# Kernel optimization log

Measured on AMD Instinct MI355X. Metric: run time of the kernel, lower is better.

Reference implementation:

```python
import jax, jax.numpy as jnp
import numpy as np

NEG_SLOPE = 0.2


def _gat_layer(x, W, a_src, a_dst, b, src, dst, n_nodes, heads, dim):
    # x: [N, F_in]; W: [F_in, heads*dim]
    h = (x @ W).reshape(n_nodes, heads, dim)            # [N,H,D]
    e_src = (h * a_src).sum(-1)                          # [N,H]
    e_dst = (h * a_dst).sum(-1)                          # [N,H]
    e = jax.nn.leaky_relu(e_src[src] + e_dst[dst], NEG_SLOPE)  # [E,H]
    # edge softmax over incoming edges of each target node
    m = jax.ops.segment_max(e, dst, num_segments=n_nodes)      # [N,H]
    ex = jnp.exp(e - m[dst])
    denom = jax.ops.segment_sum(ex, dst, num_segments=n_nodes)  # [N,H]
    alpha = ex / denom[dst]                              # [E,H]
    out = jax.ops.segment_sum(h[src] * alpha[:, :, None], dst,
                              num_segments=n_nodes)      # [N,H,D]
    return out.reshape(n_nodes, heads * dim) + b


def setup_inputs() -> dict:
    key = jax.random.key(0)
    ks = jax.random.split(key, 10)
    N, E, F_in = 100000, 1600000, 300
    x = jax.random.normal(ks[0], (N, F_in), dtype=jnp.float32)
    edge_index = jax.random.randint(ks[1], (2, E), 0, N, dtype=jnp.int64)
    s = 0.1
    return {
        'x': x,
        'edge_index': edge_index,
        'W1': jax.random.normal(ks[2], (F_in, 64), jnp.float32) * s,
        'att_src1': jax.random.normal(ks[3], (8, 8), jnp.float32) * s,
        'att_dst1': jax.random.normal(ks[4], (8, 8), jnp.float32) * s,
        'b1': jax.random.normal(ks[5], (64,), jnp.float32) * s,
        'W2': jax.random.normal(ks[6], (64, 64), jnp.float32) * s,
        'att_src2': jax.random.normal(ks[7], (1, 64), jnp.float32) * s,
        'att_dst2': jax.random.normal(ks[8], (1, 64), jnp.float32) * s,
        'b2': jax.random.normal(ks[9], (64,), jnp.float32) * s,
    }


def reference(x, edge_index, W1, att_src1, att_dst1, b1, W2, att_src2, att_dst2, b2):
    N = x.shape[0]
    # add self-loops (PyG GATConv default)
    loop = jnp.arange(N, dtype=edge_index.dtype)
    src = jnp.concatenate([edge_index[0], loop])
    dst = jnp.concatenate([edge_index[1], loop])
    # dropout p=0.6 is identity in eval mode
    h = _gat_layer(x, W1, att_src1, att_dst1, b1, src, dst, N, 8, 8)    # [N,64]
    h = jax.nn.elu(h)
    h = _gat_layer(h, W2, att_src2, att_dst2, b2, src, dst, N, 1, 64)   # [N,64]
    return jax.nn.log_softmax(h, axis=1)
```

## Files before the change

### kernel.cpp

```cpp
#include <hip/hip_runtime.h>
#include <math.h>

using short8  = __attribute__((ext_vector_type(8))) short;
using ushort8 = __attribute__((ext_vector_type(8))) unsigned short;
using f32x4   = __attribute__((ext_vector_type(4))) float;

#define NBLKS 512
#define BPAD  800
#define EB 8

__device__ __forceinline__ unsigned short f2bf(float f) {
    unsigned u = __float_as_uint(f);
    unsigned r = u + 0x7FFF + ((u >> 16) & 1);
    return (unsigned short)(r >> 16);
}
__device__ __forceinline__ float bf2f(unsigned short v) {
    return __uint_as_float((unsigned)v << 16);
}


__global__ void detect64_kernel(const int* __restrict__ ei, int E, int* __restrict__ flag) {
    __shared__ int any;
    if (threadIdx.x == 0) any = 0;
    __syncthreads();
    for (int i = threadIdx.x; i < 1024; i += 256) {
        if (ei[2 * i + 1] != 0) { any = 1; break; }
    }
    __syncthreads();
    if (threadIdx.x == 0) *flag = (any ? 0 : 1);
}


__global__ __launch_bounds__(256) void binA_kernel(
    const int* __restrict__ ei, int E, int N, const int* __restrict__ flag,
    int nbuck, int* __restrict__ hist, int chunk) {
    __shared__ int lh[BPAD];
    for (int i = threadIdx.x; i < nbuck; i += 256) lh[i] = 0;
    __syncthreads();
    int is64 = *flag;
    int Etot = E + N;
    int beg = blockIdx.x * chunk, end = min(Etot, beg + chunk);
    for (int i = beg + threadIdx.x; i < end; i += 256) {
        int d = (i < E) ? (is64 ? ei[2 * (E + i)] : ei[E + i]) : (i - E);
        atomicAdd(&lh[d >> 7], 1);
    }
    __syncthreads();
    for (int i = threadIdx.x; i < nbuck; i += 256) hist[blockIdx.x * BPAD + i] = lh[i];
}

__global__ void scanBlocks_kernel(int* __restrict__ hist, int nbuck, int* __restrict__ bucketTotal) {
    int bin = blockIdx.x * 256 + threadIdx.x;
    if (bin >= nbuck) return;
    int run = 0;
    for (int b = 0; b < NBLKS; b++) {
        int v = hist[b * BPAD + bin];
        hist[b * BPAD + bin] = run;
        run += v;
    }
    bucketTotal[bin] = run;
}

__global__ void scanBucket_kernel(const int* __restrict__ bucketTotal, int nbuck,
                                  int* __restrict__ bucketBase) {
    __shared__ int s[1024];
    int t = threadIdx.x;
    int v = (t < nbuck) ? bucketTotal[t] : 0;
    s[t] = v;
    __syncthreads();
    for (int off = 1; off < 1024; off <<= 1) {
        int x = (t >= off) ? s[t - off] : 0;
        __syncthreads();
        s[t] += x;
        __syncthreads();
    }
    if (t < nbuck) bucketBase[t] = s[t] - v;
    if (t == nbuck - 1) bucketBase[nbuck] = s[t];
}

__global__ __launch_bounds__(256) void binB_kernel(
    const int* __restrict__ ei, int E, int N, const int* __restrict__ flag,
    int nbuck, const int* __restrict__ hist, const int* __restrict__ bucketBase,
    int* __restrict__ tmp, int chunk) {
    __shared__ int cur[BPAD];
    for (int i = threadIdx.x; i < nbuck; i += 256)
        cur[i] = bucketBase[i] + hist[blockIdx.x * BPAD + i];
    __syncthreads();
    int is64 = *flag;
    int Etot = E + N;
    int beg = blockIdx.x * chunk, end = min(Etot, beg + chunk);
    for (int i = beg + threadIdx.x; i < end; i += 256) {
        int s, d;
        if (i < E) {
            if (is64) { s = ei[2 * i]; d = ei[2 * (E + i)]; }
            else      { s = ei[i];     d = ei[E + i]; }
        } else { s = i - E; d = i - E; }
        int pos = atomicAdd(&cur[d >> 7], 1);
        tmp[pos] = ((d & 127) << 17) | s;
    }
}

__global__ __launch_bounds__(256) void binC_kernel(
    const int* __restrict__ tmp, const int* __restrict__ bucketBase, int nbuck,
    int N, int Etot, int* __restrict__ rowptr, int* __restrict__ col) {
    __shared__ int lh[128];
    __shared__ int cur[128];
    int g = blockIdx.x;
    int t = threadIdx.x;
    int beg = bucketBase[g], end = bucketBase[g + 1];
    if (t < 128) lh[t] = 0;
    __syncthreads();
    for (int i = beg + t; i < end; i += 256) atomicAdd(&lh[tmp[i] >> 17], 1);
    __syncthreads();
    int c = (t < 128) ? lh[t] : 0;
    for (int off = 1; off < 128; off <<= 1) {
        int x = 0;
        if (t < 128 && t >= off) x = lh[t - off];
        __syncthreads();
        if (t < 128) lh[t] += x;
        __syncthreads();
    }
    if (t < 128) {
        int excl = lh[t] - c;
        cur[t] = beg + excl;
        int node = g * 128 + t;
        if (node < N) rowptr[node] = beg + excl;
    }
    if (g == 0 && t == 0) rowptr[N] = Etot;
    if (g == 0 && t < 16) col[Etot + t] = 0;
    __syncthreads();
    for (int i = beg + t; i < end; i += 256) {
        int v = tmp[i];
        int pos = atomicAdd(&cur[v >> 17], 1);
        col[pos] = v & 0x1FFFF;
    }
}


__global__ __launch_bounds__(256) void gemm1_mfma_kernel(
    const float* __restrict__ x, const float* __restrict__ W,
    const float* __restrict__ asrc, const float* __restrict__ adst,
    unsigned short* __restrict__ hbf, float* __restrict__ es, float* __restrict__ ed, int N) {
    __shared__ __align__(16) unsigned short A_lds[128 * 40];
    __shared__ __align__(16) unsigned short B_lds[64 * 40];
    const int tx = threadIdx.x;
    const int wv = tx >> 6;
    const int lane = tx & 63;
    const int l15 = lane & 15;
    const int quad = lane >> 4;
    const int rowBase = blockIdx.x * 128;

    f32x4 acc[2][4];
#pragma unroll
    for (int rt = 0; rt < 2; rt++)
#pragma unroll
        for (int ct = 0; ct < 4; ct++) acc[rt][ct] = (f32x4){0.f, 0.f, 0.f, 0.f};

    const int kq = tx & 7;
    const int r0 = tx >> 3;
    const int colB = tx & 63;
    const int kkb = (tx >> 6) * 8;

    for (int k0 = 0; k0 < 320; k0 += 32) {
        bool kvalid = (k0 + kq * 4 + 4 <= 300);
#pragma unroll
        for (int p = 0; p < 4; p++) {
            int row = p * 32 + r0;
            int grow = rowBase + row;
            float4 v = make_float4(0.f, 0.f, 0.f, 0.f);
            if (kvalid && grow < N) v = *(const float4*)&x[(size_t)grow * 300 + k0 + kq * 4];
            *(ushort4*)&A_lds[row * 40 + kq * 4] =
                make_ushort4(f2bf(v.x), f2bf(v.y), f2bf(v.z), f2bf(v.w));
        }
        {
            unsigned short t0, t1, t2, t3, t4, t5, t6, t7;
            float v;
            v = (k0 + kkb + 0 < 300) ? W[(size_t)(k0 + kkb + 0) * 64 + colB] : 0.f; t0 = f2bf(v);
            v = (k0 + kkb + 1 < 300) ? W[(size_t)(k0 + kkb + 1) * 64 + colB] : 0.f; t1 = f2bf(v);
            v = (k0 + kkb + 2 < 300) ? W[(size_t)(k0 + kkb + 2) * 64 + colB] : 0.f; t2 = f2bf(v);
            v = (k0 + kkb + 3 < 300) ? W[(size_t)(k0 + kkb + 3) * 64 + colB] : 0.f; t3 = f2bf(v);
            v = (k0 + kkb + 4 < 300) ? W[(size_t)(k0 + kkb + 4) * 64 + colB] : 0.f; t4 = f2bf(v);
            v = (k0 + kkb + 5 < 300) ? W[(size_t)(k0 + kkb + 5) * 64 + colB] : 0.f; t5 = f2bf(v);
            v = (k0 + kkb + 6 < 300) ? W[(size_t)(k0 + kkb + 6) * 64 + colB] : 0.f; t6 = f2bf(v);
            v = (k0 + kkb + 7 < 300) ? W[(size_t)(k0 + kkb + 7) * 64 + colB] : 0.f; t7 = f2bf(v);
            *(ushort4*)&B_lds[colB * 40 + kkb]     = make_ushort4(t0, t1, t2, t3);
            *(ushort4*)&B_lds[colB * 40 + kkb + 4] = make_ushort4(t4, t5, t6, t7);
        }
        __syncthreads();
        short8 af[2], bfr[4];
#pragma unroll
        for (int rt = 0; rt < 2; rt++)
            af[rt] = *(const short8*)&A_lds[(wv * 32 + rt * 16 + l15) * 40 + quad * 8];
#pragma unroll
        for (int ct = 0; ct < 4; ct++)
            bfr[ct] = *(const short8*)&B_lds[(ct * 16 + l15) * 40 + quad * 8];
#pragma unroll
        for (int rt = 0; rt < 2; rt++)
#pragma unroll
            for (int ct = 0; ct < 4; ct++)
                acc[rt][ct] = __builtin_amdgcn_mfma_f32_16x16x32_bf16(af[rt], bfr[ct], acc[rt][ct], 0, 0, 0);
        __syncthreads();
    }

    float as_v[4], ad_v[4];
#pragma unroll
    for (int ct = 0; ct < 4; ct++) {
        as_v[ct] = asrc[ct * 16 + l15];
        ad_v[ct] = adst[ct * 16 + l15];
    }
#pragma unroll
    for (int rt = 0; rt < 2; rt++) {
#pragma unroll
        for (int reg = 0; reg < 4; reg++) {
            int row = rowBase + wv * 32 + rt * 16 + quad * 4 + reg;
            bool ok = (row < N);
#pragma unroll
            for (int ct = 0; ct < 4; ct++) {
                float v = acc[rt][ct][reg];
                if (ok) hbf[(size_t)row * 64 + ct * 16 + l15] = f2bf(v);
                float ps = v * as_v[ct];
                float pd = v * ad_v[ct];
                ps += __shfl_xor(ps, 1); ps += __shfl_xor(ps, 2); ps += __shfl_xor(ps, 4);
                pd += __shfl_xor(pd, 1); pd += __shfl_xor(pd, 2); pd += __shfl_xor(pd, 4);
                if ((lane & 7) == 0 && ok) {
                    int head = 2 * ct + ((lane >> 3) & 1);
                    es[row * 8 + head] = ps;
                    ed[row * 8 + head] = pd;
                }
            }
        }
    }
}


__global__ __launch_bounds__(256) void gemm2_mfma_kernel(
    const unsigned short* __restrict__ xin, const float* __restrict__ W,
    const float* __restrict__ asrc, const float* __restrict__ adst,
    unsigned short* __restrict__ hbf, float* __restrict__ es, float* __restrict__ ed, int N) {
    __shared__ __align__(16) unsigned short A_lds[128 * 72];
    __shared__ __align__(16) unsigned short B_lds[64 * 72];
    const int tx = threadIdx.x;
    const int wv = tx >> 6;
    const int lane = tx & 63;
    const int l15 = lane & 15;
    const int quad = lane >> 4;
    const int rowBase = blockIdx.x * 128;

    f32x4 acc[2][4];
#pragma unroll
    for (int rt = 0; rt < 2; rt++)
#pragma unroll
        for (int ct = 0; ct < 4; ct++) acc[rt][ct] = (f32x4){0.f, 0.f, 0.f, 0.f};

    {
        int colB = tx & 63;
        int kk = (tx >> 6) * 16;
#pragma unroll
        for (int j = 0; j < 16; j++)
            B_lds[colB * 72 + kk + j] = f2bf(W[(size_t)(kk + j) * 64 + colB]);
    }
    {
        int kq = tx & 7, r0 = tx >> 3;
        const ushort8 z = (ushort8){0, 0, 0, 0, 0, 0, 0, 0};
#pragma unroll
        for (int p = 0; p < 4; p++) {
            int row = p * 32 + r0;
            int grow = rowBase + row;
            ushort8 v = z;
            if (grow < N) v = *(const ushort8*)&xin[(size_t)grow * 64 + kq * 8];
            *(ushort8*)&A_lds[row * 72 + kq * 8] = v;
        }
    }
    __syncthreads();
#pragma unroll
    for (int c = 0; c < 2; c++) {
        short8 af[2], bfr[4];
#pragma unroll
        for (int rt = 0; rt < 2; rt++)
            af[rt] = *(const short8*)&A_lds[(wv * 32 + rt * 16 + l15) * 72 + quad * 8 + c * 32];
#pragma unroll
        for (int ct = 0; ct < 4; ct++)
            bfr[ct] = *(const short8*)&B_lds[(ct * 16 + l15) * 72 + quad * 8 + c * 32];
#pragma unroll
        for (int rt = 0; rt < 2; rt++)
#pragma unroll
            for (int ct = 0; ct < 4; ct++)
                acc[rt][ct] = __builtin_amdgcn_mfma_f32_16x16x32_bf16(af[rt], bfr[ct], acc[rt][ct], 0, 0, 0);
    }

    float as_v[4], ad_v[4];
#pragma unroll
    for (int ct = 0; ct < 4; ct++) {
        as_v[ct] = asrc[ct * 16 + l15];
        ad_v[ct] = adst[ct * 16 + l15];
    }
#pragma unroll
    for (int rt = 0; rt < 2; rt++) {
#pragma unroll
        for (int reg = 0; reg < 4; reg++) {
            int row = rowBase + wv * 32 + rt * 16 + quad * 4 + reg;
            bool ok = (row < N);
            float ps = 0.f, pd = 0.f;
#pragma unroll
            for (int ct = 0; ct < 4; ct++) {
                float v = acc[rt][ct][reg];
                if (ok) hbf[(size_t)row * 64 + ct * 16 + l15] = f2bf(v);
                ps = fmaf(v, as_v[ct], ps);
                pd = fmaf(v, ad_v[ct], pd);
            }
            ps += __shfl_xor(ps, 1); ps += __shfl_xor(ps, 2);
            ps += __shfl_xor(ps, 4); ps += __shfl_xor(ps, 8);
            pd += __shfl_xor(pd, 1); pd += __shfl_xor(pd, 2);
            pd += __shfl_xor(pd, 4); pd += __shfl_xor(pd, 8);
            if (l15 == 0 && ok) { es[row] = ps; ed[row] = pd; }
        }
    }
}


__global__ __launch_bounds__(256) void agg1f_kernel(
    const int* __restrict__ rowptr, const int* __restrict__ col,
    const unsigned short* __restrict__ hbf, const float* __restrict__ es,
    const float* __restrict__ ed, const float* __restrict__ b,
    unsigned int* __restrict__ outbf, int N) {
    int node = blockIdx.x * 4 + (threadIdx.x >> 6);
    int lane = threadIdx.x & 63;
    if (node >= N) return;
    int half = lane >> 5, fl = lane & 31;
    int f0 = fl * 2, hh = fl >> 2;
    int beg = rowptr[node], end = rowptr[node + 1];
    float edv = ed[node * 8 + hh];
    float acc0 = 0.f, acc1 = 0.f, lsum = 0.f;
    for (int i = beg; i < end; i += 16) {
        int ei_[EB], ss[EB];
        float ev[EB];
        unsigned hp[EB];
#pragma unroll
        for (int j = 0; j < EB; j++) ei_[j] = i + 2 * j + half;
#pragma unroll
        for (int j = 0; j < EB; j++) ss[j] = col[ei_[j]];
#pragma unroll
        for (int j = 0; j < EB; j++) ev[j] = es[ss[j] * 8 + hh];
#pragma unroll
        for (int j = 0; j < EB; j++) hp[j] = *(const unsigned*)&hbf[(size_t)ss[j] * 64 + f0];
#pragma unroll
        for (int j = 0; j < EB; j++) {
            float e = ev[j] + edv;
            e = (e > 0.f) ? e : 0.2f * e;
            float wj = __expf(fminf(e, 30.f));
            wj = (ei_[j] < end) ? wj : 0.f;
            lsum += wj;
            float lo = __uint_as_float(hp[j] << 16);
            float hi = __uint_as_float(hp[j] & 0xFFFF0000u);
            acc0 = fmaf(wj, lo, acc0);
            acc1 = fmaf(wj, hi, acc1);
        }
    }
    acc0 += __shfl_xor(acc0, 32);
    acc1 += __shfl_xor(acc1, 32);
    lsum += __shfl_xor(lsum, 32);
    float rinv = 1.f / lsum;
    float o0 = acc0 * rinv + b[f0];
    float o1 = acc1 * rinv + b[f0 + 1];
    o0 = (o0 > 0.f) ? o0 : expm1f(o0);
    o1 = (o1 > 0.f) ? o1 : expm1f(o1);
    if (half == 0) {
        unsigned pk = (unsigned)f2bf(o0) | ((unsigned)f2bf(o1) << 16);
        outbf[((size_t)node * 64 + f0) >> 1] = pk;
    }
}

__global__ __launch_bounds__(256) void agg2f_kernel(
    const int* __restrict__ rowptr, const int* __restrict__ col,
    const unsigned short* __restrict__ hbf, const float* __restrict__ es,
    const float* __restrict__ ed, const float* __restrict__ b,
    float* __restrict__ out, int N) {
    int node = blockIdx.x * 4 + (threadIdx.x >> 6);
    int lane = threadIdx.x & 63;
    if (node >= N) return;
    int half = lane >> 5, fl = lane & 31;
    int f0 = fl * 2;
    int beg = rowptr[node], end = rowptr[node + 1];
    float edv = ed[node];
    float acc0 = 0.f, acc1 = 0.f, lsum = 0.f;
    for (int i = beg; i < end; i += 16) {
        int ei_[EB], ss[EB];
        float ev[EB];
        unsigned hp[EB];
#pragma unroll
        for (int j = 0; j < EB; j++) ei_[j] = i + 2 * j + half;
#pragma unroll
        for (int j = 0; j < EB; j++) ss[j] = col[ei_[j]];
#pragma unroll
        for (int j = 0; j < EB; j++) ev[j] = es[ss[j]];
#pragma unroll
        for (int j = 0; j < EB; j++) hp[j] = *(const unsigned*)&hbf[(size_t)ss[j] * 64 + f0];
#pragma unroll
        for (int j = 0; j < EB; j++) {
            float e = ev[j] + edv;
            e = (e > 0.f) ? e : 0.2f * e;
            float wj = __expf(fminf(e, 30.f));
            wj = (ei_[j] < end) ? wj : 0.f;
            lsum += wj;
            float lo = __uint_as_float(hp[j] << 16);
            float hi = __uint_as_float(hp[j] & 0xFFFF0000u);
            acc0 = fmaf(wj, lo, acc0);
            acc1 = fmaf(wj, hi, acc1);
        }
    }
    acc0 += __shfl_xor(acc0, 32);
    acc1 += __shfl_xor(acc1, 32);
    lsum += __shfl_xor(lsum, 32);
    float rinv = 1.f / lsum;
    float o0 = acc0 * rinv + b[f0];
    float o1 = acc1 * rinv + b[f0 + 1];
    float M = fmaxf(o0, o1);
    M = fmaxf(M, __shfl_xor(M, 1));  M = fmaxf(M, __shfl_xor(M, 2));
    M = fmaxf(M, __shfl_xor(M, 4));  M = fmaxf(M, __shfl_xor(M, 8));
    M = fmaxf(M, __shfl_xor(M, 16));
    float se = __expf(o0 - M) + __expf(o1 - M);
    se += __shfl_xor(se, 1);  se += __shfl_xor(se, 2);
    se += __shfl_xor(se, 4);  se += __shfl_xor(se, 8);
    se += __shfl_xor(se, 16);
    float ls = logf(se);
    if (half == 0) {
        float2 r = make_float2(o0 - M - ls, o1 - M - ls);
        *(float2*)&out[(size_t)node * 64 + f0] = r;
    }
}


extern "C" void kernel_launch(void* const* d_in, const int* in_sizes, int n_in,
                              void* d_out, int out_size, void* d_ws, size_t ws_size,
                              hipStream_t stream) {
    const float* x   = (const float*)d_in[0];
    const int*   ei  = (const int*)d_in[1];
    const float* W1  = (const float*)d_in[2];
    const float* as1 = (const float*)d_in[3];
    const float* ad1 = (const float*)d_in[4];
    const float* b1  = (const float*)d_in[5];
    const float* W2  = (const float*)d_in[6];
    const float* as2 = (const float*)d_in[7];
    const float* ad2 = (const float*)d_in[8];
    const float* b2  = (const float*)d_in[9];
    const int N = in_sizes[0] / 300;
    const int E = in_sizes[1] / 2;
    const int Etot = E + N;
    const int nbuck = (N + 127) >> 7;
    (void)n_in; (void)out_size; (void)ws_size;

    char* w = (char*)d_ws;
    auto alloc = [&](size_t bytes) -> char* {
        char* p = w;
        w += (bytes + 255) & ~(size_t)255;
        return p;
    };
    int*   flag        = (int*)alloc(256);
    int*   hist        = (int*)alloc((size_t)NBLKS * BPAD * 4);
    int*   bucketTotal = (int*)alloc((size_t)(BPAD + 1) * 4);
    int*   bucketBase  = (int*)alloc((size_t)(BPAD + 1) * 4);
    int*   tmp         = (int*)alloc((size_t)(Etot + 16) * 4);
    int*   rowptr      = (int*)alloc((size_t)(N + 1) * 4);
    int*   col         = (int*)alloc((size_t)(Etot + 16) * 4);
    unsigned short* h1  = (unsigned short*)alloc((size_t)N * 64 * 2);
    unsigned short* h1p = (unsigned short*)alloc((size_t)N * 64 * 2);
    float* es1         = (float*)alloc((size_t)N * 8 * 4);
    float* ed1         = (float*)alloc((size_t)N * 8 * 4);
    float* es2         = (float*)alloc((size_t)N * 4);
    float* ed2         = (float*)alloc((size_t)N * 4);
    unsigned short* h2 = h1;

    detect64_kernel<<<1, 256, 0, stream>>>(ei, E, flag);

    int chunk = (Etot + NBLKS - 1) / NBLKS;
    binA_kernel<<<NBLKS, 256, 0, stream>>>(ei, E, N, flag, nbuck, hist, chunk);
    scanBlocks_kernel<<<(nbuck + 255) / 256, 256, 0, stream>>>(hist, nbuck, bucketTotal);
    scanBucket_kernel<<<1, 1024, 0, stream>>>(bucketTotal, nbuck, bucketBase);
    binB_kernel<<<NBLKS, 256, 0, stream>>>(ei, E, N, flag, nbuck, hist, bucketBase, tmp, chunk);
    binC_kernel<<<nbuck, 256, 0, stream>>>(tmp, bucketBase, nbuck, N, Etot, rowptr, col);

    gemm1_mfma_kernel<<<(N + 127) / 128, 256, 0, stream>>>(x, W1, as1, ad1, h1, es1, ed1, N);
    agg1f_kernel<<<(N + 3) / 4, 256, 0, stream>>>(rowptr, col, h1, es1, ed1, b1,
                                                  (unsigned int*)h1p, N);
    gemm2_mfma_kernel<<<(N + 127) / 128, 256, 0, stream>>>(h1p, W2, as2, ad2, h2, es2, ed2, N);
    agg2f_kernel<<<(N + 3) / 4, 256, 0, stream>>>(rowptr, col, h2, es2, ed2, b2, (float*)d_out, N);
}
```

Baseline: 439.3 us.

## Stream x directly to MFMA registers and preload whole W1 in LDS

The first-layer GEMM now loads all of W1 into shared memory once as bf16, with a padded stride. Each wave loads its own 16 rows of x straight from global memory into registers, with a one-step software prefetch. It converts them with packed bf16 conversion and feeds the MFMA without an A-tile in LDS or per-step barriers. The block is doubled to 512 threads (8 waves of 16 rows each), and the aggregation kernels clamp out-of-range edge indices to avoid reading past the row. This targets LDS staging and synchronisation overhead in the x-bandwidth-bound GEMM, at the cost of more LDS per block and a larger W1 preload per block.

```diff
diff --git a/kernel.cpp b/kernel.cpp
--- a/kernel.cpp
+++ b/kernel.cpp
@@ -8,6 +8,7 @@
 #define NBLKS 512
 #define BPAD  800
 #define EB 8
+#define BSTR 328
 
 __device__ __forceinline__ unsigned short f2bf(float f) {
     unsigned u = __float_as_uint(f);
@@ -16,6 +17,14 @@
 }
 __device__ __forceinline__ float bf2f(unsigned short v) {
     return __uint_as_float((unsigned)v << 16);
+}
+__device__ __forceinline__ unsigned cvt2(float lo, float hi) {
+    unsigned r;
+    asm("v_cvt_pk_bf16_f32 %0, %1, %2" : "=v"(r) : "v"(lo), "v"(hi));
+    return r;
+}
+__device__ __forceinline__ float4 loadA(const float* __restrict__ p, int k) {
+    return (k + 4 <= 300) ? *(const float4*)(p + k) : make_float4(0.f, 0.f, 0.f, 0.f);
 }
 
 
@@ -136,12 +145,11 @@
 }
 
 
-__global__ __launch_bounds__(256) void gemm1_mfma_kernel(
+__global__ __launch_bounds__(512) void gemm1_mfma_kernel(
     const float* __restrict__ x, const float* __restrict__ W,
     const float* __restrict__ asrc, const float* __restrict__ adst,
     unsigned short* __restrict__ hbf, float* __restrict__ es, float* __restrict__ ed, int N) {
-    __shared__ __align__(16) unsigned short A_lds[128 * 40];
-    __shared__ __align__(16) unsigned short B_lds[64 * 40];
+    __shared__ __align__(16) unsigned short B_lds[64 * BSTR];
     const int tx = threadIdx.x;
     const int wv = tx >> 6;
     const int lane = tx & 63;
@@ -149,56 +157,49 @@
     const int quad = lane >> 4;
     const int rowBase = blockIdx.x * 128;
 
-    f32x4 acc[2][4];
-#pragma unroll
-    for (int rt = 0; rt < 2; rt++)
-#pragma unroll
-        for (int ct = 0; ct < 4; ct++) acc[rt][ct] = (f32x4){0.f, 0.f, 0.f, 0.f};
-
-    const int kq = tx & 7;
-    const int r0 = tx >> 3;
-    const int colB = tx & 63;
-    const int kkb = (tx >> 6) * 8;
-
+    {
+        int colB = tx & 63;
+        int kb0 = (tx >> 6) * 40;
+#pragma unroll
+        for (int j = 0; j < 40; j++) {
+            int k = kb0 + j;
+            float v = (k < 300) ? W[(size_t)k * 64 + colB] : 0.f;
+            B_lds[colB * BSTR + k] = f2bf(v);
+        }
+    }
+    __syncthreads();
+
+    f32x4 acc[4];
+#pragma unroll
+    for (int ct = 0; ct < 4; ct++) acc[ct] = (f32x4){0.f, 0.f, 0.f, 0.f};
+
+    const int myrow = rowBase + wv * 16 + l15;
+    const float* xr = x + (size_t)min(myrow, N - 1) * 300;
+    const int kb = quad * 8;
+
+    float4 c0 = loadA(xr, kb);
+    float4 c1 = loadA(xr, kb + 4);
+#pragma unroll
     for (int k0 = 0; k0 < 320; k0 += 32) {
-        bool kvalid = (k0 + kq * 4 + 4 <= 300);
-#pragma unroll
-        for (int p = 0; p < 4; p++) {
-            int row = p * 32 + r0;
-            int grow = rowBase + row;
-            float4 v = make_float4(0.f, 0.f, 0.f, 0.f);
-            if (kvalid && grow < N) v = *(const float4*)&x[(size_t)grow * 300 + k0 + kq * 4];
-            *(ushort4*)&A_lds[row * 40 + kq * 4] =
-                make_ushort4(f2bf(v.x), f2bf(v.y), f2bf(v.z), f2bf(v.w));
-        }
-        {
-            unsigned short t0, t1, t2, t3, t4, t5, t6, t7;
-            float v;
-            v = (k0 + kkb + 0 < 300) ? W[(size_t)(k0 + kkb + 0) * 64 + colB] : 0.f; t0 = f2bf(v);
-            v = (k0 + kkb + 1 < 300) ? W[(size_t)(k0 + kkb + 1) * 64 + colB] : 0.f; t1 = f2bf(v);
-            v = (k0 + kkb + 2 < 300) ? W[(size_t)(k0 + kkb + 2) * 64 + colB] : 0.f; t2 = f2bf(v);
-            v = (k0 + kkb + 3 < 300) ? W[(size_t)(k0 + kkb + 3) * 64 + colB] : 0.f; t3 = f2bf(v);
-            v = (k0 + kkb + 4 < 300) ? W[(size_t)(k0 + kkb + 4) * 64 + colB] : 0.f; t4 = f2bf(v);
-            v = (k0 + kkb + 5 < 300) ? W[(size_t)(k0 + kkb + 5) * 64 + colB] : 0.f; t5 = f2bf(v);
-            v = (k0 + kkb + 6 < 300) ? W[(size_t)(k0 + kkb + 6) * 64 + colB] : 0.f; t6 = f2bf(v);
-            v = (k0 + kkb + 7 < 300) ? W[(size_t)(k0 + kkb + 7) * 64 + colB] : 0.f; t7 = f2bf(v);
-            *(ushort4*)&B_lds[colB * 40 + kkb]     = make_ushort4(t0, t1, t2, t3);
-            *(ushort4*)&B_lds[colB * 40 + kkb + 4] = make_ushort4(t4, t5, t6, t7);
-        }
-        __syncthreads();
-        short8 af[2], bfr[4];
-#pragma unroll
-        for (int rt = 0; rt < 2; rt++)
-            af[rt] = *(const short8*)&A_lds[(wv * 32 + rt * 16 + l15) * 40 + quad * 8];
-#pragma unroll
-        for (int ct = 0; ct < 4; ct++)
-            bfr[ct] = *(const short8*)&B_lds[(ct * 16 + l15) * 40 + quad * 8];
-#pragma unroll
-        for (int rt = 0; rt < 2; rt++)
-#pragma unroll
-            for (int ct = 0; ct < 4; ct++)
-                acc[rt][ct] = __builtin_amdgcn_mfma_f32_16x16x32_bf16(af[rt], bfr[ct], acc[rt][ct], 0, 0, 0);
-        __syncthreads();
+        float4 n0, n1;
+        if (k0 < 288) {
+            n0 = loadA(xr, k0 + 32 + kb);
+            n1 = loadA(xr, k0 + 36 + kb);
+        } else {
+            n0 = make_float4(0.f, 0.f, 0.f, 0.f);
+            n1 = make_float4(0.f, 0.f, 0.f, 0.f);
+        }
+        union { unsigned u[4]; short8 s; } cv;
+        cv.u[0] = cvt2(c0.x, c0.y);
+        cv.u[1] = cvt2(c0.z, c0.w);
+        cv.u[2] = cvt2(c1.x, c1.y);
+        cv.u[3] = cvt2(c1.z, c1.w);
+#pragma unroll
+        for (int ct = 0; ct < 4; ct++) {
+            short8 bfr = *(const short8*)&B_lds[(ct * 16 + l15) * BSTR + k0 + kb];
+            acc[ct] = __builtin_amdgcn_mfma_f32_16x16x32_bf16(cv.s, bfr, acc[ct], 0, 0, 0);
+        }
+        c0 = n0; c1 = n1;
     }
 
     float as_v[4], ad_v[4];
@@ -208,24 +209,21 @@
         ad_v[ct] = adst[ct * 16 + l15];
     }
 #pragma unroll
-    for (int rt = 0; rt < 2; rt++) {
-#pragma unroll
-        for (int reg = 0; reg < 4; reg++) {
-            int row = rowBase + wv * 32 + rt * 16 + quad * 4 + reg;
-            bool ok = (row < N);
-#pragma unroll
-            for (int ct = 0; ct < 4; ct++) {
-                float v = acc[rt][ct][reg];
-                if (ok) hbf[(size_t)row * 64 + ct * 16 + l15] = f2bf(v);
-                float ps = v * as_v[ct];
-                float pd = v * ad_v[ct];
-                ps += __shfl_xor(ps, 1); ps += __shfl_xor(ps, 2); ps += __shfl_xor(ps, 4);
-                pd += __shfl_xor(pd, 1); pd += __shfl_xor(pd, 2); pd += __shfl_xor(pd, 4);
-                if ((lane & 7) == 0 && ok) {
-                    int head = 2 * ct + ((lane >> 3) & 1);
-                    es[row * 8 + head] = ps;
-                    ed[row * 8 + head] = pd;
-                }
+    for (int reg = 0; reg < 4; reg++) {
+        int row = rowBase + wv * 16 + quad * 4 + reg;
+        bool ok = (row < N);
+#pragma unroll
+        for (int ct = 0; ct < 4; ct++) {
+            float v = acc[ct][reg];
+            if (ok) hbf[(size_t)row * 64 + ct * 16 + l15] = f2bf(v);
+            float ps = v * as_v[ct];
+            float pd = v * ad_v[ct];
+            ps += __shfl_xor(ps, 1); ps += __shfl_xor(ps, 2); ps += __shfl_xor(ps, 4);
+            pd += __shfl_xor(pd, 1); pd += __shfl_xor(pd, 2); pd += __shfl_xor(pd, 4);
+            if ((lane & 7) == 0 && ok) {
+                int head = 2 * ct + ((lane >> 3) & 1);
+                es[row * 8 + head] = ps;
+                ed[row * 8 + head] = pd;
             }
         }
     }
@@ -337,7 +335,7 @@
 #pragma unroll
         for (int j = 0; j < EB; j++) ei_[j] = i + 2 * j + half;
 #pragma unroll
-        for (int j = 0; j < EB; j++) ss[j] = col[ei_[j]];
+        for (int j = 0; j < EB; j++) ss[j] = col[(ei_[j] < end) ? ei_[j] : beg];
 #pragma unroll
         for (int j = 0; j < EB; j++) ev[j] = es[ss[j] * 8 + hh];
 #pragma unroll
@@ -389,7 +387,7 @@
 #pragma unroll
         for (int j = 0; j < EB; j++) ei_[j] = i + 2 * j + half;
 #pragma unroll
-        for (int j = 0; j < EB; j++) ss[j] = col[ei_[j]];
+        for (int j = 0; j < EB; j++) ss[j] = col[(ei_[j] < end) ? ei_[j] : beg];
 #pragma unroll
         for (int j = 0; j < EB; j++) ev[j] = es[ss[j]];
 #pragma unroll
@@ -478,7 +476,7 @@
     binB_kernel<<<NBLKS, 256, 0, stream>>>(ei, E, N, flag, nbuck, hist, bucketBase, tmp, chunk);
     binC_kernel<<<nbuck, 256, 0, stream>>>(tmp, bucketBase, nbuck, N, Etot, rowptr, col);
 
-    gemm1_mfma_kernel<<<(N + 127) / 128, 256, 0, stream>>>(x, W1, as1, ad1, h1, es1, ed1, N);
+    gemm1_mfma_kernel<<<(N + 127) / 128, 512, 0, stream>>>(x, W1, as1, ad1, h1, es1, ed1, N);
     agg1f_kernel<<<(N + 3) / 4, 256, 0, stream>>>(rowptr, col, h1, es1, ed1, b1,
                                                   (unsigned int*)h1p, N);
     gemm2_mfma_kernel<<<(N + 127) / 128, 256, 0, stream>>>(h1p, W2, as2, ad2, h2, es2, ed2, N);
```

Measured after the change: 469.0 us. +6.8%, slower.
